# Performance work log

Measured on AMD Instinct MI355X. Metric: run time of the kernel, lower is better.

Reference implementation:

```python
import jax, jax.numpy as jnp
import numpy as np
import math

def _ln(x, g, b, eps=1e-5):
    mu = x.mean(-1, keepdims=True)
    var = ((x - mu) ** 2).mean(-1, keepdims=True)
    return (x - mu) / jnp.sqrt(var + eps) * g + b

def _mha(x, in_w, in_b, out_w, out_b, nh):
    # torch nn.MultiheadAttention (batch_first, eval): q,k,v chunks of in_proj
    Bn, Nn, Dm = x.shape
    hd = Dm // nh
    q, k, v = jnp.split(x @ in_w.T + in_b, 3, axis=-1)
    sp = lambda t: t.reshape(Bn, Nn, nh, hd).transpose(0, 2, 1, 3)
    q, k, v = sp(q), sp(k), sp(v)
    a = jax.nn.softmax(jnp.einsum('bhid,bhjd->bhij', q, k) / math.sqrt(hd), axis=-1)
    y = jnp.einsum('bhij,bhjd->bhid', a, v).transpose(0, 2, 1, 3).reshape(Bn, Nn, Dm)
    return y @ out_w.T + out_b

def setup_inputs():
    key = jax.random.key(0)
    ks = iter(jax.random.split(key, 40))
    nrm = lambda shape: jax.random.normal(next(ks), shape, jnp.float32) * 0.02
    B, T, C, H, W = 2, 32, 3, 64, 64
    D, P, nL, nS = 512, 8, 6, 3
    N = (H // P) ** 2
    z = lambda *s: jnp.zeros(s, jnp.float32)
    o = lambda *s: jnp.ones(s, jnp.float32)
    return dict(
        x=jax.random.normal(next(ks), (B, T, C, H, W), jnp.float32),
        patch_w=nrm((D, C * P * P)), patch_b=z(D),
        tok_ln_g=o(D), tok_ln_b=z(D),
        spatial_pos=nrm((1, 1, N, D)), temporal_pos=nrm((1, T, 1, D)),
        snorm_g=o(D), snorm_b=z(D),
        sa_in_w=nrm((nS, 3 * D, D)), sa_in_b=z(nS, 3 * D),
        sa_out_w=nrm((nS, D, D)), sa_out_b=z(nS, D),
        ln1_g=o(nL, D), ln1_b=z(nL, D),
        kqv_w=nrm((nL, 3 * D, D)), kqv_b=z(nL, 3 * D),
        proj_w=nrm((nL, D, D)), proj_b=z(nL, D),
        ln2_g=o(nL, D), ln2_b=z(nL, D),
        fc_w=nrm((nL, 4 * D, D)), fc_b=z(nL, 4 * D),
        cproj_w=nrm((nL, D, 4 * D)), cproj_b=z(nL, D),
        lnf_g=o(D), lnf_b=z(D),
        th_w1=nrm((D // 2, D)), th_b1=z(D // 2), th_w2=nrm((1, D // 2)), th_b2=z(1),
        sh_w1=nrm((D // 2, D)), sh_b1=z(D // 2), sh_w2=nrm((1, D // 2)), sh_b2=z(1),
        pf_w1=nrm((D // 2, D)), pf_b1=z(D // 2), pf_w2=nrm((1, D // 2)), pf_b2=z(1),
    )

def reference(x, patch_w, patch_b, tok_ln_g, tok_ln_b, spatial_pos, temporal_pos,
              snorm_g, snorm_b, sa_in_w, sa_in_b, sa_out_w, sa_out_b,
              ln1_g, ln1_b, kqv_w, kqv_b, proj_w, proj_b, ln2_g, ln2_b,
              fc_w, fc_b, cproj_w, cproj_b, lnf_g, lnf_b,
              th_w1, th_b1, th_w2, th_b2, sh_w1, sh_b1, sh_w2, sh_b2,
              pf_w1, pf_b1, pf_w2, pf_b2):
    B, T, C, H, W = x.shape
    D = patch_w.shape[0]
    P = int(math.isqrt(patch_w.shape[1] // C))
    Hn, Wn = H // P, W // P
    N = Hn * Wn
    # Conv3d kernel=(1,P,P), stride=(1,P,P) == per-frame patchify + matmul
    patches = x.reshape(B, T, C, Hn, P, Wn, P).transpose(0, 1, 3, 5, 2, 4, 6).reshape(B, T, N, C * P * P)
    tok = _ln(patches @ patch_w.T + patch_b, tok_ln_g, tok_ln_b)
    tok = tok + spatial_pos + temporal_pos[:, :T]
    # per-frame spatial attention: identical math per frame -> batch over B*T
    s = tok.reshape(B * T, N, D)
    for i in range(sa_in_w.shape[0]):
        s = s + _mha(_ln(s, snorm_g, snorm_b), sa_in_w[i], sa_in_b[i], sa_out_w[i], sa_out_b[i], nh=4)
    L = T * N
    hid = s.reshape(B, L, D)
    nh = 8
    hd = D // nh
    mask = jnp.tril(jnp.ones((L, L), bool))  # causal over T*N tokens
    for i in range(kqv_w.shape[0]):
        a_in = _ln(hid, ln1_g[i], ln1_b[i])
        k, q, v = jnp.split(a_in @ kqv_w[i].T + kqv_b[i], 3, axis=-1)  # torch split order: k, q, v
        sp = lambda t: t.reshape(B, L, nh, hd).transpose(0, 2, 1, 3)
        q, k, v = sp(q), sp(k), sp(v)
        att = jnp.einsum('bhid,bhjd->bhij', q, k) / math.sqrt(hd)
        att = jax.nn.softmax(jnp.where(mask, att, -jnp.inf), axis=-1)
        y = jnp.einsum('bhij,bhjd->bhid', att, v).transpose(0, 2, 1, 3).reshape(B, L, D)
        hid = hid + y @ proj_w[i].T + proj_b[i]
        m_in = _ln(hid, ln2_g[i], ln2_b[i])
        h = jax.nn.gelu(m_in @ fc_w[i].T + fc_b[i], approximate=False)
        hid = hid + h @ cproj_w[i].T + cproj_b[i]
    hid = _ln(hid, lnf_g, lnf_b).reshape(B, T, N, D)
    head = lambda zz, w1, b1, w2, b2: jax.nn.leaky_relu(zz @ w1.T + b1, 0.2) @ w2.T + b2
    tf = hid.mean(axis=2)  # [B, T, D]
    temporal_score = head(tf[:, -1], th_w1, th_b1, th_w2, th_b2)  # [B, 1] (last timestep, full lengths)
    spatial_score = head(hid.mean(axis=1).mean(axis=1), sh_w1, sh_b1, sh_w2, sh_b2)
    per_frame_scores = head(tf, pf_w1, pf_b1, pf_w2, pf_b2)  # [B, T, 1]
    final_score = temporal_score + spatial_score + per_frame_scores.mean(axis=1)
    return (temporal_score, spatial_score, per_frame_scores, final_score)
```

## Files before the change

kernel.cpp:

```cpp
#include <hip/hip_runtime.h>
#include <hip/hip_bf16.h>
#include <math.h>

#define MTOK 4096

typedef __bf16 bf16x8 __attribute__((ext_vector_type(8)));
typedef float f32x4 __attribute__((ext_vector_type(4)));

__device__ __forceinline__ ushort f2bf(float f){
  __hip_bfloat16 h = __float2bfloat16(f);
  return *reinterpret_cast<ushort*>(&h);
}
__device__ __forceinline__ float bf2f(ushort u){
  return __uint_as_float(((uint)u) << 16);
}
__device__ __forceinline__ void gload_lds16(const void* g, void* l){
  __builtin_amdgcn_global_load_lds((__attribute__((address_space(1))) void*)(void*)g,
                                   (__attribute__((address_space(3))) void*)l, 16, 0, 0);
}

__device__ __forceinline__ float blockReduceSum(float v, float* red){
  #pragma unroll
  for (int off = 32; off; off >>= 1) v += __shfl_down(v, off, 64);
  int lane = threadIdx.x & 63, wid = threadIdx.x >> 6;
  __syncthreads();
  if (lane == 0) red[wid] = v;
  __syncthreads();
  float r = 0.f;
  int nw = blockDim.x >> 6;
  for (int i = 0; i < nw; i++) r += red[i];
  return r;
}
__device__ __forceinline__ float rowMax16(float v){
  #pragma unroll
  for (int m = 8; m; m >>= 1) v = fmaxf(v, __shfl_xor(v, m, 64));
  return v;
}
__device__ __forceinline__ float rowSum16(float v){
  #pragma unroll
  for (int m = 8; m; m >>= 1) v += __shfl_xor(v, m, 64);
  return v;
}

__global__ __launch_bounds__(256) void cvt_w_kernel(
    const float* __restrict__ src, ushort* __restrict__ dst, int n)
{
  int i = (blockIdx.x * 256 + threadIdx.x) * 8;
  float4 a = *(const float4*)(src + i);
  float4 b = *(const float4*)(src + i + 4);
  uint4 o;
  o.x = (uint)f2bf(a.x) | ((uint)f2bf(a.y) << 16);
  o.y = (uint)f2bf(a.z) | ((uint)f2bf(a.w) << 16);
  o.z = (uint)f2bf(b.x) | ((uint)f2bf(b.y) << 16);
  o.w = (uint)f2bf(b.z) | ((uint)f2bf(b.w) << 16);
  *(uint4*)(dst + i) = o;
}

#define OFF_PATCH 0u
#define OFF_SAIN  98304u
#define OFF_SAOUT 2457600u
#define OFF_KQV   3244032u
#define OFF_PROJ  7962624u
#define OFF_FC    9535488u
#define OFF_CPROJ 15826944u
#define W_TOTAL   22118400u
__global__ __launch_bounds__(256) void cvt_all_kernel(
    const float* __restrict__ pw, const float* __restrict__ sain,
    const float* __restrict__ saout, const float* __restrict__ kqv,
    const float* __restrict__ proj, const float* __restrict__ fc,
    const float* __restrict__ cproj, ushort* __restrict__ dst)
{
  int blk = blockIdx.x;
  const float* src; size_t off;
  if      (blk <    48){ src = pw;    off = OFF_PATCH; }
  else if (blk <  1200){ src = sain;  off = OFF_SAIN;  blk -= 48;   }
  else if (blk <  1584){ src = saout; off = OFF_SAOUT; blk -= 1200; }
  else if (blk <  3888){ src = kqv;   off = OFF_KQV;   blk -= 1584; }
  else if (blk <  4656){ src = proj;  off = OFF_PROJ;  blk -= 3888; }
  else if (blk <  7728){ src = fc;    off = OFF_FC;    blk -= 4656; }
  else                 { src = cproj; off = OFF_CPROJ; blk -= 7728; }
  size_t si = (size_t)blk*2048 + threadIdx.x*8;
  float4 a = *(const float4*)(src + si);
  float4 b = *(const float4*)(src + si + 4);
  uint4 o;
  o.x = (uint)f2bf(a.x) | ((uint)f2bf(a.y) << 16);
  o.y = (uint)f2bf(a.z) | ((uint)f2bf(a.w) << 16);
  o.z = (uint)f2bf(b.x) | ((uint)f2bf(b.y) << 16);
  o.w = (uint)f2bf(b.z) | ((uint)f2bf(b.w) << 16);
  *(uint4*)(dst + off + si) = o;
}

__global__ __launch_bounds__(256) void im2col_kernel(
    const float* __restrict__ x, ushort* __restrict__ Pm)
{
  int idx = blockIdx.x*256 + threadIdx.x;
  int m = idx / 24, e8 = idx % 24;
  int b = m >> 11, t = (m >> 6) & 31, n = m & 63;
  int hn = n >> 3, wn = n & 7;
  int c = e8 >> 3, ph = e8 & 7;
  const float* src = x + (((size_t)(b*32 + t)*3 + c)*64 + hn*8 + ph)*64 + wn*8;
  float4 a = *(const float4*)src;
  float4 bq = *(const float4*)(src + 4);
  uint4 o;
  o.x = (uint)f2bf(a.x) | ((uint)f2bf(a.y) << 16);
  o.y = (uint)f2bf(a.z) | ((uint)f2bf(a.w) << 16);
  o.z = (uint)f2bf(bq.x) | ((uint)f2bf(bq.y) << 16);
  o.w = (uint)f2bf(bq.z) | ((uint)f2bf(bq.w) << 16);
  *(uint4*)(Pm + (size_t)m*192 + e8*8) = o;
}

__global__ __launch_bounds__(256) void ln_pos_kernel(
    const float* __restrict__ in, float* __restrict__ out,
    const float* __restrict__ g, const float* __restrict__ b,
    const float* __restrict__ spos, const float* __restrict__ tpos)
{
  int r = blockIdx.x*4 + (threadIdx.x >> 6);
  int lane = threadIdx.x & 63;
  int n = r & 63, t = (r >> 6) & 31;
  const float* row = in + (size_t)r*512 + lane*8;
  float4 v0 = *(const float4*)row;
  float4 v1 = *(const float4*)(row + 4);
  float s = v0.x+v0.y+v0.z+v0.w+v1.x+v1.y+v1.z+v1.w;
  float q = v0.x*v0.x+v0.y*v0.y+v0.z*v0.z+v0.w*v0.w+v1.x*v1.x+v1.y*v1.y+v1.z*v1.z+v1.w*v1.w;
  #pragma unroll
  for (int m = 1; m < 64; m <<= 1){ s += __shfl_xor(s, m, 64); q += __shfl_xor(q, m, 64); }
  float mu = s*(1.f/512.f);
  float inv = rsqrtf(q*(1.f/512.f) - mu*mu + 1e-5f);
  const float* gp = g + lane*8;
  const float* bp = b + lane*8;
  const float* sp = spos + n*512 + lane*8;
  const float* tp = tpos + t*512 + lane*8;
  float* op = out + (size_t)r*512 + lane*8;
  #pragma unroll
  for (int e = 0; e < 2; e++){
    float4 vv = e ? v1 : v0;
    float4 gg = *(const float4*)(gp + e*4);
    float4 bb = *(const float4*)(bp + e*4);
    float4 ss = *(const float4*)(sp + e*4);
    float4 tt = *(const float4*)(tp + e*4);
    float4 oo;
    oo.x = (vv.x-mu)*inv*gg.x + bb.x + ss.x + tt.x;
    oo.y = (vv.y-mu)*inv*gg.y + bb.y + ss.y + tt.y;
    oo.z = (vv.z-mu)*inv*gg.z + bb.z + ss.z + tt.z;
    oo.w = (vv.w-mu)*inv*gg.w + bb.w + ss.w + tt.w;
    *(float4*)(op + e*4) = oo;
  }
}

__global__ __launch_bounds__(256) void ln_bf16_kernel(
    const float* __restrict__ in, ushort* __restrict__ out,
    const float* __restrict__ g, const float* __restrict__ b)
{
  int r = blockIdx.x*4 + (threadIdx.x >> 6);
  int lane = threadIdx.x & 63;
  const float* row = in + (size_t)r*512 + lane*8;
  float4 v0 = *(const float4*)row;
  float4 v1 = *(const float4*)(row + 4);
  float s = v0.x+v0.y+v0.z+v0.w+v1.x+v1.y+v1.z+v1.w;
  float q = v0.x*v0.x+v0.y*v0.y+v0.z*v0.z+v0.w*v0.w+v1.x*v1.x+v1.y*v1.y+v1.z*v1.z+v1.w*v1.w;
  #pragma unroll
  for (int m = 1; m < 64; m <<= 1){ s += __shfl_xor(s, m, 64); q += __shfl_xor(q, m, 64); }
  float mu = s*(1.f/512.f);
  float inv = rsqrtf(q*(1.f/512.f) - mu*mu + 1e-5f);
  float4 g0 = *(const float4*)(g + lane*8);
  float4 g1 = *(const float4*)(g + lane*8 + 4);
  float4 b0 = *(const float4*)(b + lane*8);
  float4 b1 = *(const float4*)(b + lane*8 + 4);
  uint4 o;
  o.x = (uint)f2bf((v0.x-mu)*inv*g0.x + b0.x) | ((uint)f2bf((v0.y-mu)*inv*g0.y + b0.y) << 16);
  o.y = (uint)f2bf((v0.z-mu)*inv*g0.z + b0.z) | ((uint)f2bf((v0.w-mu)*inv*g0.w + b0.w) << 16);
  o.z = (uint)f2bf((v1.x-mu)*inv*g1.x + b1.x) | ((uint)f2bf((v1.y-mu)*inv*g1.y + b1.y) << 16);
  o.w = (uint)f2bf((v1.z-mu)*inv*g1.z + b1.z) | ((uint)f2bf((v1.w-mu)*inv*g1.w + b1.w) << 16);
  *(uint4*)(out + (size_t)r*512 + lane*8) = o;
}

template<int BM, int BN, bool GELU, bool BF16OUT>
__global__ __launch_bounds__(256) void gemm2_kernel(
    const ushort* __restrict__ X, const ushort* __restrict__ Wb,
    const float* __restrict__ bias, const float* __restrict__ res,
    void* __restrict__ Yv, int M, int Nn, int K)
{
  constexpr int WROWS = (BN == 128) ? 2 : 4;
  constexpr int WM = BM / WROWS;
  constexpr int FM = WM / 16;
  constexpr int FN = 4;
  __shared__ __attribute__((aligned(16))) char smem[2*(BM+BN)*128];
  char* Xs0 = smem;
  char* Ws0 = smem + BM*128;
  char* Xs1 = smem + (BM+BN)*128;
  char* Ws1 = Xs1 + BM*128;
  int tid = threadIdx.x, lane = tid & 63, wv = tid >> 6;
  int bm = blockIdx.y * BM, bn = blockIdx.x * BN;
  int wm, wn;
  if (BN == 128){ wm = (wv >> 1) * WM; wn = (wv & 1) * 64; }
  else          { wm = wv * WM;        wn = 0; }

  f32x4 acc[FM][FN];
  #pragma unroll
  for (int i = 0; i < FM; i++)
    #pragma unroll
    for (int j = 0; j < FN; j++){ f32x4 z = {0.f,0.f,0.f,0.f}; acc[i][j] = z; }

  int rowoff = wv*8 + (lane >> 3);
  int colsrc = ((lane & 7) ^ (lane >> 3)) * 16;

  auto stage = [&](char* Xd, char* Wd, int k0){
    #pragma unroll
    for (int i = 0; i < BM/32; i++){
      int row = i*32 + rowoff;
      gload_lds16((const char*)(X + (size_t)(bm + row)*K + k0) + colsrc,
                  Xd + (i*32 + wv*8)*128);
    }
    #pragma unroll
    for (int i = 0; i < BN/32; i++){
      int row = i*32 + rowoff;
      gload_lds16((const char*)(Wb + (size_t)(bn + row)*K + k0) + colsrc,
                  Wd + (i*32 + wv*8)*128);
    }
  };

  stage(Xs0, Ws0, 0);
  __syncthreads();
  int nt = K >> 6;
  for (int t = 0; t < nt; t++){
    char* Xc = (t & 1) ? Xs1 : Xs0;
    char* Wc = (t & 1) ? Ws1 : Ws0;
    if (t + 1 < nt) stage((t & 1) ? Xs0 : Xs1, (t & 1) ? Ws0 : Ws1, (t+1)*64);
    #pragma unroll
    for (int kc = 0; kc < 2; kc++){
      bf16x8 a[FM], b[FN];
      #pragma unroll
      for (int f = 0; f < FM; f++){
        int ra = wm + f*16 + (lane & 15);
        a[f] = *(const bf16x8*)(Xc + ra*128 + ((kc*64 + (lane>>4)*16) ^ ((ra & 7) << 4)));
      }
      #pragma unroll
      for (int f = 0; f < FN; f++){
        int rb = wn + f*16 + (lane & 15);
        b[f] = *(const bf16x8*)(Wc + rb*128 + ((kc*64 + (lane>>4)*16) ^ ((rb & 7) << 4)));
      }
      #pragma unroll
      for (int i = 0; i < FM; i++)
        #pragma unroll
        for (int j = 0; j < FN; j++)
          acc[i][j] = __builtin_amdgcn_mfma_f32_16x16x32_bf16(a[i], b[j], acc[i][j], 0, 0, 0);
    }
    __syncthreads();
  }
  int col0 = lane & 15;
  float bv[FN];
  #pragma unroll
  for (int fn = 0; fn < FN; fn++) bv[fn] = bias[bn + wn + fn*16 + col0];
  #pragma unroll
  for (int fm = 0; fm < FM; fm++){
    #pragma unroll
    for (int r = 0; r < 4; r++){
      int m = bm + wm + fm*16 + (lane >> 4)*4 + r;
      #pragma unroll
      for (int fn = 0; fn < FN; fn++){
        int n = bn + wn + fn*16 + col0;
        float v = acc[fm][fn][r] + bv[fn];
        if (res) v += res[(size_t)m*Nn + n];
        if (GELU) v = 0.5f * v * (1.f + erff(v * 0.70710678118654752440f));
        if (BF16OUT) ((ushort*)Yv)[(size_t)m*Nn + n] = f2bf(v);
        else         ((float*) Yv)[(size_t)m*Nn + n] = v;
      }
    }
  }
}

__global__ __launch_bounds__(256) void spatial_attn_mfma_kernel(
    const ushort* __restrict__ qkv, ushort* __restrict__ y)
{
  __shared__ __attribute__((aligned(16))) char Ks[64*256];
  __shared__ __attribute__((aligned(16))) char Vt[128*128];
  __shared__ __attribute__((aligned(16))) char Ps[64*128];
  int bt = blockIdx.x, h = blockIdx.y;
  int tid = threadIdx.x, lane = tid & 63, w = tid >> 6;
  const ushort* base = qkv + (size_t)bt*64*1536 + (size_t)h*128;
  const float scale = 0.08838834764831845f;

  int qrow = w*16 + (lane & 15);
  bf16x8 qa[4];
  #pragma unroll
  for (int kc = 0; kc < 4; kc++)
    qa[kc] = *(const bf16x8*)(base + (size_t)qrow*1536 + kc*32 + (lane>>4)*8);

  #pragma unroll
  for (int i = 0; i < 4; i++){
    int row = w*16 + i*4 + (lane >> 4);
    const char* src = (const char*)(base + (size_t)row*1536 + 512) + (((lane & 15) ^ (row & 15)) * 16);
    char* dst = Ks + (w*16 + i*4)*256;
    gload_lds16(src, dst);
  }
  {
    int vj = (tid & 31) * 2;
    int d0 = (tid >> 5) * 16;
    const ushort* v0p = base + (size_t)vj*1536 + 1024 + d0;
    const ushort* v1p = v0p + 1536;
    uint4 a0 = *(const uint4*)(v0p);
    uint4 a1 = *(const uint4*)(v0p + 8);
    uint4 b0 = *(const uint4*)(v1p);
    uint4 b1 = *(const uint4*)(v1p + 8);
    uint av[8] = {a0.x, a0.y, a0.z, a0.w, a1.x, a1.y, a1.z, a1.w};
    uint bv[8] = {b0.x, b0.y, b0.z, b0.w, b1.x, b1.y, b1.z, b1.w};
    int cb = 4 * (tid & 31);
    #pragma unroll
    for (int e = 0; e < 8; e++){
      int dl = d0 + e*2, dh = dl + 1;
      uint vlo = (av[e] & 0xffffu) | ((bv[e] & 0xffffu) << 16);
      uint vhi = (av[e] >> 16) | (bv[e] & 0xffff0000u);
      *(uint*)(Vt + dl*128 + (cb ^ ((dl & 7) << 4))) = vlo;
      *(uint*)(Vt + dh*128 + (cb ^ ((dh & 7) << 4))) = vhi;
    }
  }
  __syncthreads();

  f32x4 zero4 = {0.f,0.f,0.f,0.f};
  f32x4 accS[4];
  __builtin_amdgcn_s_setprio(1);
  #pragma unroll
  for (int jt = 0; jt < 4; jt++){
    accS[jt] = zero4;
    #pragma unroll
    for (int kc = 0; kc < 4; kc++){
      int krow = jt*16 + (lane & 15);
      bf16x8 kb = *(const bf16x8*)(Ks + krow*256 + ((kc*64 + (lane>>4)*16) ^ ((krow & 15) << 4)));
      accS[jt] = __builtin_amdgcn_mfma_f32_16x16x32_bf16(qa[kc], kb, accS[jt], 0, 0, 0);
    }
  }
  __builtin_amdgcn_s_setprio(0);
  float l_sum[4];
  #pragma unroll
  for (int r = 0; r < 4; r++){
    float mx = fmaxf(fmaxf(accS[0][r], accS[1][r]), fmaxf(accS[2][r], accS[3][r]));
    mx = rowMax16(mx);
    int prow = w*16 + (lane>>4)*4 + r;
    int swz = (prow & 7) << 4;
    char* pbase = Ps + prow*128;
    float ps = 0.f;
    #pragma unroll
    for (int jt = 0; jt < 4; jt++){
      float p = __expf((accS[jt][r] - mx) * scale);
      ushort pb = f2bf(p);
      *(ushort*)(pbase + ((2*(jt*16 + (lane & 15))) ^ swz)) = pb;
      ps += bf2f(pb);
    }
    l_sum[r] = rowSum16(ps);
  }
  bf16x8 pa[2];
  #pragma unroll
  for (int kc2 = 0; kc2 < 2; kc2++){
    int prow = w*16 + (lane & 15);
    pa[kc2] = *(const bf16x8*)(Ps + prow*128 + ((kc2*64 + (lane>>4)*16) ^ ((prow & 7) << 4)));
  }
  f32x4 o[8];
  __builtin_amdgcn_s_setprio(1);
  #pragma unroll
  for (int dt = 0; dt < 8; dt++){
    o[dt] = zero4;
    #pragma unroll
    for (int kc2 = 0; kc2 < 2; kc2++){
      int vrow = dt*16 + (lane & 15);
      bf16x8 vb = *(const bf16x8*)(Vt + vrow*128 + ((kc2*64 + (lane>>4)*16) ^ ((vrow & 7) << 4)));
      o[dt] = __builtin_amdgcn_mfma_f32_16x16x32_bf16(pa[kc2], vb, o[dt], 0, 0, 0);
    }
  }
  __builtin_amdgcn_s_setprio(0);
  #pragma unroll
  for (int r = 0; r < 4; r++){
    float invl = 1.f / l_sum[r];
    int token = bt*64 + w*16 + (lane>>4)*4 + r;
    ushort* yrow = y + (size_t)token*512 + h*128;
    #pragma unroll
    for (int dt = 0; dt < 8; dt++)
      yrow[dt*16 + (lane & 15)] = f2bf(o[dt][r] * invl);
  }
}

__global__ __launch_bounds__(256) void temporal_attn_split_kernel(
    const ushort* __restrict__ qkv, ushort* __restrict__ Op, float* __restrict__ ml)
{
  __shared__ __attribute__((aligned(16))) char Ks[64*128];
  __shared__ __attribute__((aligned(16))) char Vt[64*128];
  __shared__ __attribute__((aligned(16))) char Ps[64*128];
  int id = blockIdx.x;
  int bh = id & 15;
  int rest = id >> 4;
  int qt = 31 - (rest >> 1);
  int half = rest & 1;
  int b = bh >> 3, h = bh & 7;
  int tid = threadIdx.x, lane = tid & 63, w = tid >> 6;
  const ushort* base = qkv + (size_t)(b*2048)*1536 + h*64;

  int nk = qt + 1;
  int ktm = (nk + 1) >> 1;
  int kt0 = half ? ktm : 0;
  int kt1 = half ? nk : ktm;

  int qrow = qt*64 + w*16 + (lane & 15);
  bf16x8 qa[2];
  #pragma unroll
  for (int kc = 0; kc < 2; kc++)
    qa[kc] = *(const bf16x8*)(base + (size_t)qrow*1536 + 512 + kc*32 + (lane>>4)*8);

  f32x4 zero4 = {0.f,0.f,0.f,0.f};
  f32x4 o[4];
  float m_old[4], l_sum[4];
  #pragma unroll
  for (int dt = 0; dt < 4; dt++) o[dt] = zero4;
  #pragma unroll
  for (int r = 0; r < 4; r++){ m_old[r] = -1e30f; l_sum[r] = 0.f; }

  int kcolsrc = ((lane & 7) ^ (lane >> 3)) * 16;
  int vj  = (tid & 31) * 2;
  int vd0 = (tid >> 5) * 8;
  int vcb = 4 * (tid & 31);

  for (int kt = kt0; kt < kt1; kt++){
    __syncthreads();
    #pragma unroll
    for (int i = 0; i < 2; i++){
      int row = w*16 + i*8 + (lane >> 3);
      gload_lds16((const char*)(base + (size_t)(kt*64 + row)*1536) + kcolsrc,
                  Ks + (w*16 + i*8)*128);
    }
    {
      const ushort* v0p = base + (size_t)(kt*64 + vj)*1536 + 1024 + vd0;
      const ushort* v1p = v0p + 1536;
      uint4 a0 = *(const uint4*)v0p;
      uint4 b0 = *(const uint4*)v1p;
      uint av[4] = {a0.x, a0.y, a0.z, a0.w};
      uint bv[4] = {b0.x, b0.y, b0.z, b0.w};
      #pragma unroll
      for (int e = 0; e < 4; e++){
        int dl = vd0 + e*2, dh = dl + 1;
        uint vlo = (av[e] & 0xffffu) | ((bv[e] & 0xffffu) << 16);
        uint vhi = (av[e] >> 16) | (bv[e] & 0xffff0000u);
        *(uint*)(Vt + dl*128 + (vcb ^ ((dl & 7) << 4))) = vlo;
        *(uint*)(Vt + dh*128 + (vcb ^ ((dh & 7) << 4))) = vhi;
      }
    }
    __syncthreads();

    f32x4 accS[4];
    __builtin_amdgcn_s_setprio(1);
    #pragma unroll
    for (int jt = 0; jt < 4; jt++){
      accS[jt] = zero4;
      #pragma unroll
      for (int kc = 0; kc < 2; kc++){
        int krow = jt*16 + (lane & 15);
        bf16x8 kb = *(const bf16x8*)(Ks + krow*128 + ((kc*64 + (lane>>4)*16) ^ ((krow & 7) << 4)));
        accS[jt] = __builtin_amdgcn_mfma_f32_16x16x32_bf16(qa[kc], kb, accS[jt], 0, 0, 0);
      }
    }
    __builtin_amdgcn_s_setprio(0);
    if (kt == qt){
      #pragma unroll
      for (int jt = 0; jt < 4; jt++){
        int gj = kt*64 + jt*16 + (lane & 15);
        #pragma unroll
        for (int r = 0; r < 4; r++){
          int gi = qt*64 + w*16 + (lane>>4)*4 + r;
          if (gj > gi) accS[jt][r] = -1e30f;
        }
      }
    }
    #pragma unroll
    for (int r = 0; r < 4; r++){
      float mloc = fmaxf(fmaxf(accS[0][r], accS[1][r]), fmaxf(accS[2][r], accS[3][r])) * 0.125f;
      mloc = rowMax16(mloc);
      float mnew = fmaxf(m_old[r], mloc);
      float corr = __expf(m_old[r] - mnew);
      int prow = w*16 + (lane>>4)*4 + r;
      int swz = (prow & 7) << 4;
      char* pbase = Ps + prow*128;
      float ps = 0.f;
      #pragma unroll
      for (int jt = 0; jt < 4; jt++){
        float p = __expf(accS[jt][r]*0.125f - mnew);
        ushort pb = f2bf(p);
        *(ushort*)(pbase + ((2*(jt*16 + (lane & 15))) ^ swz)) = pb;
        ps += bf2f(pb);
      }
      l_sum[r] = l_sum[r]*corr + ps;
      m_old[r] = mnew;
      #pragma unroll
      for (int dt = 0; dt < 4; dt++) o[dt][r] *= corr;
    }
    bf16x8 pa[2];
    #pragma unroll
    for (int kc2 = 0; kc2 < 2; kc2++){
      int prow = w*16 + (lane & 15);
      pa[kc2] = *(const bf16x8*)(Ps + prow*128 + ((kc2*64 + (lane>>4)*16) ^ ((prow & 7) << 4)));
    }
    __builtin_amdgcn_s_setprio(1);
    #pragma unroll
    for (int dt = 0; dt < 4; dt++){
      #pragma unroll
      for (int kc2 = 0; kc2 < 2; kc2++){
        int vrow = dt*16 + (lane & 15);
        bf16x8 vb = *(const bf16x8*)(Vt + vrow*128 + ((kc2*64 + (lane>>4)*16) ^ ((vrow & 7) << 4)));
        o[dt] = __builtin_amdgcn_mfma_f32_16x16x32_bf16(pa[kc2], vb, o[dt], 0, 0, 0);
      }
    }
    __builtin_amdgcn_s_setprio(0);
  }
  #pragma unroll
  for (int r = 0; r < 4; r++) l_sum[r] = rowSum16(l_sum[r]);
  size_t tokbase = (size_t)half*4096 + (size_t)b*2048;
  #pragma unroll
  for (int r = 0; r < 4; r++){
    int token = qt*64 + w*16 + (lane>>4)*4 + r;
    ushort* yrow = Op + (tokbase + token)*512 + h*64;
    #pragma unroll
    for (int dt = 0; dt < 4; dt++)
      yrow[dt*16 + (lane & 15)] = f2bf(o[dt][r]);
    if ((lane & 15) == 0){
      float* mlp = ml + ((tokbase + token)*8 + h)*2;
      mlp[0] = m_old[r];
      mlp[1] = l_sum[r];
    }
  }
}

__global__ __launch_bounds__(256) void attn_merge_kernel(
    const ushort* __restrict__ Op, const float* __restrict__ ml, ushort* __restrict__ Ef)
{
  int tok = blockIdx.x*4 + (threadIdx.x >> 6);
  int l6 = threadIdx.x & 63;
  int h = l6 >> 3, d0 = (l6 & 7)*8;
  int e = h*64 + d0;
  const float* m1p = ml + ((size_t)tok*8 + h)*2;
  const float* m2p = ml + (((size_t)4096 + tok)*8 + h)*2;
  float m1 = m1p[0], l1 = m1p[1];
  float m2 = m2p[0], l2 = m2p[1];
  float mm = fmaxf(m1, m2);
  float w1 = __expf(m1 - mm), w2 = __expf(m2 - mm);
  float inv = 1.f / (w1*l1 + w2*l2);
  uint4 a = *(const uint4*)(Op + (size_t)tok*512 + e);
  uint4 bq = *(const uint4*)(Op + ((size_t)4096 + tok)*512 + e);
  uint av[4] = {a.x, a.y, a.z, a.w};
  uint bv[4] = {bq.x, bq.y, bq.z, bq.w};
  uint ov[4];
  #pragma unroll
  for (int p = 0; p < 4; p++){
    float x0 = (w1*bf2f((ushort)(av[p] & 0xffff)) + w2*bf2f((ushort)(bv[p] & 0xffff))) * inv;
    float x1 = (w1*bf2f((ushort)(av[p] >> 16))    + w2*bf2f((ushort)(bv[p] >> 16)))    * inv;
    ov[p] = (uint)f2bf(x0) | ((uint)f2bf(x1) << 16);
  }
  uint4 o; o.x = ov[0]; o.y = ov[1]; o.z = ov[2]; o.w = ov[3];
  *(uint4*)(Ef + (size_t)tok*512 + e) = o;
}

__global__ __launch_bounds__(256) void reduce_tf_kernel(const ushort* __restrict__ hid, float* __restrict__ tf){
  int bt = blockIdx.x, tid = threadIdx.x;
  for (int d = tid; d < 512; d += 256){
    float s = 0.f;
    for (int n = 0; n < 64; n++) s += bf2f(hid[((size_t)bt*64 + n)*512 + d]);
    tf[(size_t)bt*512 + d] = s * (1.f/64.f);
  }
}

__global__ __launch_bounds__(256) void head_kernel(
    const float* __restrict__ tf,
    const float* __restrict__ th_w1, const float* __restrict__ th_b1,
    const float* __restrict__ th_w2, const float* __restrict__ th_b2,
    const float* __restrict__ sh_w1, const float* __restrict__ sh_b1,
    const float* __restrict__ sh_w2, const float* __restrict__ sh_b2,
    const float* __restrict__ pf_w1, const float* __restrict__ pf_b1,
    const float* __restrict__ pf_w2, const float* __restrict__ pf_b2,
    float* __restrict__ out)
{
  __shared__ float z[512];
  __shared__ float red[4];
  int bi = blockIdx.x, tid = threadIdx.x;
  const float *w1, *b1, *w2, *b2;
  float* dst;
  if (bi < 64){
    w1 = pf_w1; b1 = pf_b1; w2 = pf_w2; b2 = pf_b2; dst = out + 4 + bi;
    z[tid]       = tf[(size_t)bi*512 + tid];
    z[tid + 256] = tf[(size_t)bi*512 + tid + 256];
  } else if (bi < 66){
    int b = bi - 64;
    w1 = th_w1; b1 = th_b1; w2 = th_w2; b2 = th_b2; dst = out + b;
    z[tid]       = tf[(size_t)(b*32 + 31)*512 + tid];
    z[tid + 256] = tf[(size_t)(b*32 + 31)*512 + tid + 256];
  } else {
    int b = bi - 66;
    w1 = sh_w1; b1 = sh_b1; w2 = sh_w2; b2 = sh_b2; dst = out + 2 + b;
    float s0 = 0.f, s1 = 0.f;
    for (int t = 0; t < 32; t++){
      s0 += tf[(size_t)(b*32 + t)*512 + tid];
      s1 += tf[(size_t)(b*32 + t)*512 + tid + 256];
    }
    z[tid] = s0 * (1.f/32.f); z[tid + 256] = s1 * (1.f/32.f);
  }
  __syncthreads();
  float a = b1[tid];
  const float* wrow = w1 + (size_t)tid * 512;
  for (int k = 0; k < 512; k++) a = fmaf(wrow[k], z[k], a);
  a = (a > 0.f) ? a : 0.2f * a;
  float s = blockReduceSum(a * w2[tid], red);
  if (tid == 0) *dst = s + b2[0];
}

__global__ __launch_bounds__(64) void final_kernel(float* __restrict__ out){
  int b = threadIdx.x;
  if (b < 2){
    float s = 0.f;
    for (int t = 0; t < 32; t++) s += out[4 + b*32 + t];
    out[68 + b] = out[b] + out[2 + b] + s * (1.f/32.f);
  }
}

extern "C" void kernel_launch(void* const* d_in, const int* in_sizes, int n_in,
                              void* d_out, int out_size, void* d_ws, size_t ws_size,
                              hipStream_t stream)
{
  const float* x          = (const float*)d_in[0];
  const float* patch_w    = (const float*)d_in[1];
  const float* patch_b    = (const float*)d_in[2];
  const float* tok_ln_g   = (const float*)d_in[3];
  const float* tok_ln_b   = (const float*)d_in[4];
  const float* spatial_pos= (const float*)d_in[5];
  const float* temporal_pos=(const float*)d_in[6];
  const float* snorm_g    = (const float*)d_in[7];
  const float* snorm_b    = (const float*)d_in[8];
  const float* sa_in_w    = (const float*)d_in[9];
  const float* sa_in_b    = (const float*)d_in[10];
  const float* sa_out_w   = (const float*)d_in[11];
  const float* sa_out_b   = (const float*)d_in[12];
  const float* ln1_g      = (const float*)d_in[13];
  const float* ln1_b      = (const float*)d_in[14];
  const float* kqv_w      = (const float*)d_in[15];
  const float* kqv_b      = (const float*)d_in[16];
  const float* proj_w     = (const float*)d_in[17];
  const float* proj_b     = (const float*)d_in[18];
  const float* ln2_g      = (const float*)d_in[19];
  const float* ln2_b      = (const float*)d_in[20];
  const float* fc_w       = (const float*)d_in[21];
  const float* fc_b       = (const float*)d_in[22];
  const float* cproj_w    = (const float*)d_in[23];
  const float* cproj_b    = (const float*)d_in[24];
  const float* lnf_g      = (const float*)d_in[25];
  const float* lnf_b      = (const float*)d_in[26];
  const float* th_w1 = (const float*)d_in[27];
  const float* th_b1 = (const float*)d_in[28];
  const float* th_w2 = (const float*)d_in[29];
  const float* th_b2 = (const float*)d_in[30];
  const float* sh_w1 = (const float*)d_in[31];
  const float* sh_b1 = (const float*)d_in[32];
  const float* sh_w2 = (const float*)d_in[33];
  const float* sh_b2 = (const float*)d_in[34];
  const float* pf_w1 = (const float*)d_in[35];
  const float* pf_b1 = (const float*)d_in[36];
  const float* pf_w2 = (const float*)d_in[37];
  const float* pf_b2 = (const float*)d_in[38];

  float* out = (float*)d_out;
  char* p = (char*)d_ws;
  float*  A  = (float*)p;      p += (size_t)MTOK*512*4;
  ushort* Ru = (ushort*)p;     p += (size_t)MTOK*2048*2;
  ushort* Bf = (ushort*)p;     p += (size_t)MTOK*512*2;
  ushort* Ef = (ushort*)p;     p += (size_t)MTOK*512*2;
  float*  tfp = (float*)p;     p += (size_t)64*512*4;
  ushort* OpB = (ushort*)p;    p += (size_t)2*MTOK*512*2;
  float*  mlB = (float*)p;     p += (size_t)2*MTOK*8*2*4;
  ushort* Wslot = (ushort*)p;  p += (size_t)1048576*2;
  ushort* Wall = (ushort*)p;   p += (size_t)W_TOTAL*2;
  const size_t NEED_BIG = (size_t)(p - (char*)d_ws);
  float*  Pf = (float*)Ru;
  ushort* Pm = Ef;

  const bool big = (ws_size >= NEED_BIG);

  if (big){
    cvt_all_kernel<<<10800, 256, 0, stream>>>(patch_w, sa_in_w, sa_out_w, kqv_w,
                                              proj_w, fc_w, cproj_w, Wall);
  }
  auto W = [&](const float* src, size_t arena_off, size_t nelem) -> const ushort* {
    if (big) return Wall + arena_off;
    cvt_w_kernel<<<(int)(nelem/2048), 256, 0, stream>>>(src, Wslot, (int)nelem);
    return Wslot;
  };

  im2col_kernel<<<384, 256, 0, stream>>>(x, Pm);
  gemm2_kernel<64,64,false,false><<<dim3(8, 64), 256, 0, stream>>>(
      Pm, W(patch_w, OFF_PATCH, 512*192), patch_b, nullptr, Pf, MTOK, 512, 192);
  ln_pos_kernel<<<1024, 256, 0, stream>>>(Pf, A, tok_ln_g, tok_ln_b, spatial_pos, temporal_pos);

  for (int i = 0; i < 3; i++){
    ln_bf16_kernel<<<1024, 256, 0, stream>>>(A, Bf, snorm_g, snorm_b);
    gemm2_kernel<64,128,false,true><<<dim3(12, 64), 256, 0, stream>>>(
        Bf, W(sa_in_w + (size_t)i*1536*512, OFF_SAIN + (size_t)i*786432, 1536*512),
        sa_in_b + (size_t)i*1536, nullptr, Ru, MTOK, 1536, 512);
    spatial_attn_mfma_kernel<<<dim3(64, 4), 256, 0, stream>>>(Ru, Ef);
    gemm2_kernel<64,64,false,false><<<dim3(8, 64), 256, 0, stream>>>(
        Ef, W(sa_out_w + (size_t)i*512*512, OFF_SAOUT + (size_t)i*262144, 512*512),
        sa_out_b + (size_t)i*512, A, A, MTOK, 512, 512);
  }
  for (int i = 0; i < 6; i++){
    ln_bf16_kernel<<<1024, 256, 0, stream>>>(A, Bf, ln1_g + (size_t)i*512, ln1_b + (size_t)i*512);
    gemm2_kernel<64,128,false,true><<<dim3(12, 64), 256, 0, stream>>>(
        Bf, W(kqv_w + (size_t)i*1536*512, OFF_KQV + (size_t)i*786432, 1536*512),
        kqv_b + (size_t)i*1536, nullptr, Ru, MTOK, 1536, 512);
    temporal_attn_split_kernel<<<1024, 256, 0, stream>>>(Ru, OpB, mlB);
    attn_merge_kernel<<<1024, 256, 0, stream>>>(OpB, mlB, Ef);
    gemm2_kernel<64,64,false,false><<<dim3(8, 64), 256, 0, stream>>>(
        Ef, W(proj_w + (size_t)i*512*512, OFF_PROJ + (size_t)i*262144, 512*512),
        proj_b + (size_t)i*512, A, A, MTOK, 512, 512);
    ln_bf16_kernel<<<1024, 256, 0, stream>>>(A, Bf, ln2_g + (size_t)i*512, ln2_b + (size_t)i*512);
    gemm2_kernel<64,128,true,true><<<dim3(16, 64), 256, 0, stream>>>(
        Bf, W(fc_w + (size_t)i*2048*512, OFF_FC + (size_t)i*1048576, 2048*512),
        fc_b + (size_t)i*2048, nullptr, Ru, MTOK, 2048, 512);
    gemm2_kernel<64,64,false,false><<<dim3(8, 64), 256, 0, stream>>>(
        Ru, W(cproj_w + (size_t)i*512*2048, OFF_CPROJ + (size_t)i*1048576, 512*2048),
        cproj_b + (size_t)i*512, A, A, MTOK, 512, 2048);
  }
  ln_bf16_kernel<<<1024, 256, 0, stream>>>(A, Bf, lnf_g, lnf_b);
  reduce_tf_kernel<<<64, 256, 0, stream>>>(Bf, tfp);
  head_kernel<<<68, 256, 0, stream>>>(tfp, th_w1, th_b1, th_w2, th_b2,
                                      sh_w1, sh_b1, sh_w2, sh_b2,
                                      pf_w1, pf_b1, pf_w2, pf_b2, out);
  final_kernel<<<1, 64, 0, stream>>>(out);
}
```

Measured before the change: 843.5 us.

## Compute transposed S^T in temporal attention so each lane owns one query row

The temporal attention split kernel swaps the MFMA operand order so the score tile is computed transposed, which gives each lane a single query row. Row max and sum then reduce with two cross-lane xor shuffles instead of 16-lane reductions repeated for four rows, and P is written with packed 8-byte stores into a per-wave LDS slice. Output stores become vectorized ushort4 writes, and the per-row softmax state drops from four registers to one. The risk is a change in LDS bank-conflict behaviour on the new P write pattern.

Result: faster. 806.2 us (-4.4%).

```diff
diff --git a/kernel.cpp b/kernel.cpp
--- a/kernel.cpp
+++ b/kernel.cpp
@@ -383,7 +383,7 @@
 {
   __shared__ __attribute__((aligned(16))) char Ks[64*128];
   __shared__ __attribute__((aligned(16))) char Vt[64*128];
-  __shared__ __attribute__((aligned(16))) char Ps[64*128];
+  __shared__ __attribute__((aligned(16))) char Ps[4*16*128];
   int id = blockIdx.x;
   int bh = id & 15;
   int rest = id >> 4;
@@ -391,6 +391,7 @@
   int half = rest & 1;
   int b = bh >> 3, h = bh & 7;
   int tid = threadIdx.x, lane = tid & 63, w = tid >> 6;
+  int g = lane >> 4, q = lane & 15;
   const ushort* base = qkv + (size_t)(b*2048)*1536 + h*64;
 
   int nk = qt + 1;
@@ -398,24 +399,24 @@
   int kt0 = half ? ktm : 0;
   int kt1 = half ? nk : ktm;
 
-  int qrow = qt*64 + w*16 + (lane & 15);
-  bf16x8 qa[2];
+  int qrow = qt*64 + w*16 + q;
+  bf16x8 qb[2];
   #pragma unroll
   for (int kc = 0; kc < 2; kc++)
-    qa[kc] = *(const bf16x8*)(base + (size_t)qrow*1536 + 512 + kc*32 + (lane>>4)*8);
+    qb[kc] = *(const bf16x8*)(base + (size_t)qrow*1536 + 512 + kc*32 + g*8);
 
   f32x4 zero4 = {0.f,0.f,0.f,0.f};
   f32x4 o[4];
-  float m_old[4], l_sum[4];
   #pragma unroll
   for (int dt = 0; dt < 4; dt++) o[dt] = zero4;
-  #pragma unroll
-  for (int r = 0; r < 4; r++){ m_old[r] = -1e30f; l_sum[r] = 0.f; }
+  float m_old = -1e30f, l_sum = 0.f;
 
   int kcolsrc = ((lane & 7) ^ (lane >> 3)) * 16;
   int vj  = (tid & 31) * 2;
   int vd0 = (tid >> 5) * 8;
   int vcb = 4 * (tid & 31);
+  char* myP = Ps + w*2048;
+  int pswz = (q & 7) << 4;
 
   for (int kt = kt0; kt < kt1; kt++){
     __syncthreads();
@@ -450,78 +451,83 @@
       accS[jt] = zero4;
       #pragma unroll
       for (int kc = 0; kc < 2; kc++){
-        int krow = jt*16 + (lane & 15);
-        bf16x8 kb = *(const bf16x8*)(Ks + krow*128 + ((kc*64 + (lane>>4)*16) ^ ((krow & 7) << 4)));
-        accS[jt] = __builtin_amdgcn_mfma_f32_16x16x32_bf16(qa[kc], kb, accS[jt], 0, 0, 0);
+        int krow = jt*16 + q;
+        bf16x8 kb = *(const bf16x8*)(Ks + krow*128 + ((kc*64 + g*16) ^ ((krow & 7) << 4)));
+        accS[jt] = __builtin_amdgcn_mfma_f32_16x16x32_bf16(kb, qb[kc], accS[jt], 0, 0, 0);
       }
     }
     __builtin_amdgcn_s_setprio(0);
     if (kt == qt){
+      int gi = qt*64 + w*16 + q;
       #pragma unroll
-      for (int jt = 0; jt < 4; jt++){
-        int gj = kt*64 + jt*16 + (lane & 15);
+      for (int jt = 0; jt < 4; jt++)
         #pragma unroll
         for (int r = 0; r < 4; r++){
-          int gi = qt*64 + w*16 + (lane>>4)*4 + r;
+          int gj = kt*64 + jt*16 + g*4 + r;
           if (gj > gi) accS[jt][r] = -1e30f;
         }
-      }
-    }
-    #pragma unroll
-    for (int r = 0; r < 4; r++){
-      float mloc = fmaxf(fmaxf(accS[0][r], accS[1][r]), fmaxf(accS[2][r], accS[3][r])) * 0.125f;
-      mloc = rowMax16(mloc);
-      float mnew = fmaxf(m_old[r], mloc);
-      float corr = __expf(m_old[r] - mnew);
-      int prow = w*16 + (lane>>4)*4 + r;
-      int swz = (prow & 7) << 4;
-      char* pbase = Ps + prow*128;
-      float ps = 0.f;
-      #pragma unroll
-      for (int jt = 0; jt < 4; jt++){
-        float p = __expf(accS[jt][r]*0.125f - mnew);
-        ushort pb = f2bf(p);
-        *(ushort*)(pbase + ((2*(jt*16 + (lane & 15))) ^ swz)) = pb;
-        ps += bf2f(pb);
-      }
-      l_sum[r] = l_sum[r]*corr + ps;
-      m_old[r] = mnew;
-      #pragma unroll
-      for (int dt = 0; dt < 4; dt++) o[dt][r] *= corr;
-    }
-    bf16x8 pa[2];
-    #pragma unroll
-    for (int kc2 = 0; kc2 < 2; kc2++){
-      int prow = w*16 + (lane & 15);
-      pa[kc2] = *(const bf16x8*)(Ps + prow*128 + ((kc2*64 + (lane>>4)*16) ^ ((prow & 7) << 4)));
-    }
+    }
+    float mloc = fmaxf(fmaxf(accS[0][0], accS[0][1]), fmaxf(accS[0][2], accS[0][3]));
+    #pragma unroll
+    for (int jt = 1; jt < 4; jt++){
+      float t2 = fmaxf(fmaxf(accS[jt][0], accS[jt][1]), fmaxf(accS[jt][2], accS[jt][3]));
+      mloc = fmaxf(mloc, t2);
+    }
+    mloc *= 0.125f;
+    mloc = fmaxf(mloc, __shfl_xor(mloc, 16, 64));
+    mloc = fmaxf(mloc, __shfl_xor(mloc, 32, 64));
+    float mnew = fmaxf(m_old, mloc);
+    float corr = __expf(m_old - mnew);
+    float ps = 0.f;
+    #pragma unroll
+    for (int jt = 0; jt < 4; jt++){
+      ushort pb0 = f2bf(__expf(accS[jt][0]*0.125f - mnew));
+      ushort pb1 = f2bf(__expf(accS[jt][1]*0.125f - mnew));
+      ushort pb2 = f2bf(__expf(accS[jt][2]*0.125f - mnew));
+      ushort pb3 = f2bf(__expf(accS[jt][3]*0.125f - mnew));
+      ps += bf2f(pb0) + bf2f(pb1) + bf2f(pb2) + bf2f(pb3);
+      uint2 wv;
+      wv.x = (uint)pb0 | ((uint)pb1 << 16);
+      wv.y = (uint)pb2 | ((uint)pb3 << 16);
+      *(uint2*)(myP + q*128 + ((jt*32 + g*8) ^ pswz)) = wv;
+    }
+    l_sum = l_sum*corr + ps;
+    m_old = mnew;
+    #pragma unroll
+    for (int dt = 0; dt < 4; dt++) o[dt] *= corr;
+
+    bf16x8 pfr[2];
+    #pragma unroll
+    for (int kc2 = 0; kc2 < 2; kc2++)
+      pfr[kc2] = *(const bf16x8*)(myP + q*128 + ((kc2*64 + g*16) ^ pswz));
     __builtin_amdgcn_s_setprio(1);
     #pragma unroll
     for (int dt = 0; dt < 4; dt++){
       #pragma unroll
       for (int kc2 = 0; kc2 < 2; kc2++){
-        int vrow = dt*16 + (lane & 15);
-        bf16x8 vb = *(const bf16x8*)(Vt + vrow*128 + ((kc2*64 + (lane>>4)*16) ^ ((vrow & 7) << 4)));
-        o[dt] = __builtin_amdgcn_mfma_f32_16x16x32_bf16(pa[kc2], vb, o[dt], 0, 0, 0);
+        int vrow = dt*16 + q;
+        bf16x8 vb = *(const bf16x8*)(Vt + vrow*128 + ((kc2*64 + g*16) ^ ((vrow & 7) << 4)));
+        o[dt] = __builtin_amdgcn_mfma_f32_16x16x32_bf16(vb, pfr[kc2], o[dt], 0, 0, 0);
       }
     }
     __builtin_amdgcn_s_setprio(0);
   }
-  #pragma unroll
-  for (int r = 0; r < 4; r++) l_sum[r] = rowSum16(l_sum[r]);
+  l_sum += __shfl_xor(l_sum, 16, 64);
+  l_sum += __shfl_xor(l_sum, 32, 64);
   size_t tokbase = (size_t)half*4096 + (size_t)b*2048;
-  #pragma unroll
-  for (int r = 0; r < 4; r++){
-    int token = qt*64 + w*16 + (lane>>4)*4 + r;
-    ushort* yrow = Op + (tokbase + token)*512 + h*64;
-    #pragma unroll
-    for (int dt = 0; dt < 4; dt++)
-      yrow[dt*16 + (lane & 15)] = f2bf(o[dt][r]);
-    if ((lane & 15) == 0){
-      float* mlp = ml + ((tokbase + token)*8 + h)*2;
-      mlp[0] = m_old[r];
-      mlp[1] = l_sum[r];
-    }
+  int token = qt*64 + w*16 + q;
+  ushort* yrow = Op + (tokbase + token)*512 + h*64;
+  #pragma unroll
+  for (int dt = 0; dt < 4; dt++){
+    ushort4 o4;
+    o4.x = f2bf(o[dt][0]); o4.y = f2bf(o[dt][1]);
+    o4.z = f2bf(o[dt][2]); o4.w = f2bf(o[dt][3]);
+    *(ushort4*)(yrow + dt*16 + g*4) = o4;
+  }
+  if (g == 0){
+    float* mlp = ml + ((tokbase + token)*8 + h)*2;
+    mlp[0] = m_old;
+    mlp[1] = l_sum;
   }
 }
 
```
